# Performance work log

Measured on AMD Instinct MI355X. Metric: run time of the kernel, lower is better.

The kernel has to match this reference:

```python
import jax, jax.numpy as jnp
import numpy as np

B, S, H, I = 2, 2048, 4096, 14336

def setup_inputs() -> dict:
    key = jax.random.key(0)
    k1, k2, k3, k4 = jax.random.split(key, 4)
    sH = 1.0 / np.sqrt(H)
    sI = 1.0 / np.sqrt(I)
    return {
        "x": jax.random.normal(k1, (B, S, H), dtype=jnp.float32),
        "w_gate": jax.random.normal(k2, (I, H), dtype=jnp.float32) * sH,
        "w_up": jax.random.normal(k3, (I, H), dtype=jnp.float32) * sH,
        "w_down": jax.random.normal(k4, (H, I), dtype=jnp.float32) * sI,
    }

def reference(x, w_gate, w_up, w_down):
    # SwiGLU gated MLP: down( silu(x @ Wg^T) * (x @ Wu^T) )
    g = jnp.einsum("bsh,ih->bsi", x, w_gate)   # [B,S,I]
    u = jnp.einsum("bsh,ih->bsi", x, w_up)     # [B,S,I]
    a = jax.nn.silu(g) * u                      # fused silu_mul
    d = jnp.einsum("bsi,hi->bsh", a, w_down)   # [B,S,H]
    return d
```

## Files before the change

kernel.cpp:

```cpp
#include <hip/hip_runtime.h>
#include <hip/hip_bf16.h>
#include <stdint.h>

typedef __bf16 bf16_t;
typedef __bf16 bf16x4 __attribute__((ext_vector_type(4)));
typedef __bf16 bf16x8 __attribute__((ext_vector_type(8)));
typedef float f32x4 __attribute__((ext_vector_type(4)));

#define LDS_CAST(p) ((__attribute__((address_space(3))) void*)(p))
#define GLB_CAST(p) ((const __attribute__((address_space(1))) void*)(p))

__device__ __forceinline__ void gl_lds16(const void* g, void* l) {
  __builtin_amdgcn_global_load_lds(GLB_CAST(g), LDS_CAST(l), 16, 0, 0);
}

#define MFMA16(a,b,c) __builtin_amdgcn_mfma_f32_16x16x32_bf16((a),(b),(c),0,0,0)
#define BARRIER() __builtin_amdgcn_s_barrier()
#define LGKM0() do { asm volatile("s_waitcnt lgkmcnt(0)" ::: "memory"); \
                     __builtin_amdgcn_sched_barrier(0); } while(0)
#define VMW(n)  asm volatile("s_waitcnt vmcnt(" #n ")" ::: "memory")

static constexpr int M_TOT = 4096, H_DIM = 4096, I_DIM = 14336;

__global__ __launch_bounds__(256)
void k_conv(const float4* __restrict__ src, bf16x4* __restrict__ dst, long n4)
{
  long stride = (long)gridDim.x * blockDim.x;
  for (long i = (long)blockIdx.x * blockDim.x + threadIdx.x; i < n4; i += stride) {
    float4 v = src[i];
    bf16x4 o;
    o[0] = (bf16_t)v.x; o[1] = (bf16_t)v.y; o[2] = (bf16_t)v.z; o[3] = (bf16_t)v.w;
    dst[i] = o;
  }
}

__global__ __launch_bounds__(512, 2)
void k_gateup8(const bf16_t* __restrict__ X, const bf16_t* __restrict__ Wg,
               const bf16_t* __restrict__ Wu, bf16_t* __restrict__ Aout)
{
  __shared__ __align__(1024) char lds[131072];
  const int tid = threadIdx.x, wave = tid >> 6, lane = tid & 63;
  const int lr = lane & 15, kg = lane >> 4;
  const int xm = ((lr >> 3) & 1) << 5;
  const int wm = wave >> 2, wn = wave & 3;

  const int bid = blockIdx.x;
  const int swz = (bid & 7) * 224 + (bid >> 3);
  const int tm = swz / 112, tn = swz % 112;

  const int srow  = tid >> 2;
  const int scolb = ((tid & 3) * 16) ^ (((tid >> 5) & 1) << 5);

  const bf16_t* gX = X  + (size_t)(tm * 256 + srow) * H_DIM + (scolb >> 1);
  const bf16_t* gG = Wg + (size_t)(tn * 128 + srow) * H_DIM + (scolb >> 1);
  const bf16_t* gU = Wu + (size_t)(tn * 128 + srow) * H_DIM + (scolb >> 1);
  const size_t xh = (size_t)128 * H_DIM;

  const int offA = (wm * 128 + lr) * 64 + ((kg * 16) ^ xm);
  const int offG = 16384 + (wn * 32 + lr) * 64 + ((kg * 16) ^ xm);
  const int offU = offG + 8192;

  const f32x4 vz = {0.f, 0.f, 0.f, 0.f};
  f32x4 accg[8][2], accu[8][2];
#pragma unroll
  for (int m = 0; m < 8; ++m)
#pragma unroll
    for (int n = 0; n < 2; ++n) { accg[m][n] = vz; accu[m][n] = vz; }

#pragma unroll
  for (int t = 0; t < 3; ++t) {
    char* lb = lds + t * 32768 + wave * 1024;
    gl_lds16(gX + t * 32,      lb);
    gl_lds16(gX + xh + t * 32, lb + 8192);
    gl_lds16(gG + t * 32,      lb + 16384);
    gl_lds16(gU + t * 32,      lb + 24576);
  }
  VMW(8); BARRIER();

  bf16x8 bg[2], bu[2];

#define G1_PHA(bb, DO_STG, sb, kc, VMWAIT)                                    \
  {                                                                           \
    bf16x8 a0[4];                                                             \
    _Pragma("unroll") for (int f = 0; f < 4; ++f)                             \
      a0[f] = *(const bf16x8*)((bb) + offA + f * 1024);                       \
    _Pragma("unroll") for (int n = 0; n < 2; ++n) {                           \
      bg[n] = *(const bf16x8*)((bb) + offG + n * 1024);                       \
      bu[n] = *(const bf16x8*)((bb) + offU + n * 1024); }                     \
    if (DO_STG) { gl_lds16(gX + (kc), (sb));                                  \
                  gl_lds16(gX + xh + (kc), (sb) + 8192); }                    \
    BARRIER(); LGKM0();                                                       \
    __builtin_amdgcn_s_setprio(1);                                            \
    _Pragma("unroll") for (int m = 0; m < 4; ++m)                             \
    _Pragma("unroll") for (int n = 0; n < 2; ++n) {                           \
      accg[m][n] = MFMA16(a0[m], bg[n], accg[m][n]);                          \
      accu[m][n] = MFMA16(a0[m], bu[n], accu[m][n]); }                        \
    __builtin_amdgcn_s_setprio(0);                                            \
    VMWAIT; BARRIER();                                                        \
  }

#define G1_PHB(bb, DO_STG, sb, kc, VMWAIT)                                    \
  {                                                                           \
    bf16x8 a1[4];                                                             \
    _Pragma("unroll") for (int f = 0; f < 4; ++f)                             \
      a1[f] = *(const bf16x8*)((bb) + offA + (f + 4) * 1024);                 \
    if (DO_STG) { gl_lds16(gG + (kc), (sb) + 16384);                          \
                  gl_lds16(gU + (kc), (sb) + 24576); }                        \
    BARRIER(); LGKM0();                                                       \
    __builtin_amdgcn_s_setprio(1);                                            \
    _Pragma("unroll") for (int m = 0; m < 4; ++m)                             \
    _Pragma("unroll") for (int n = 0; n < 2; ++n) {                           \
      accg[4 + m][n] = MFMA16(a1[m], bg[n], accg[4 + m][n]);                  \
      accu[4 + m][n] = MFMA16(a1[m], bu[n], accu[4 + m][n]); }                \
    __builtin_amdgcn_s_setprio(0);                                            \
    VMWAIT; BARRIER();                                                        \
  }

  const int NT = H_DIM / 32;
  for (int T = 0; T < NT - 3; ++T) {
    const char* bb = lds + (T & 3) * 32768;
    char* sb = lds + ((T + 3) & 3) * 32768 + wave * 1024;
    const int kc = (T + 3) * 32;
    G1_PHA(bb, true, sb, kc, VMW(8));
    G1_PHB(bb, true, sb, kc, VMW(8));
  }
  { const char* bb = lds + ((NT-3) & 3) * 32768;
    G1_PHA(bb, false, lds, 0, VMW(4)); G1_PHB(bb, false, lds, 0, VMW(4)); }
  { const char* bb = lds + ((NT-2) & 3) * 32768;
    G1_PHA(bb, false, lds, 0, VMW(0)); G1_PHB(bb, false, lds, 0, VMW(0)); }
  { const char* bb = lds + ((NT-1) & 3) * 32768;
    G1_PHA(bb, false, lds, 0, VMW(0)); G1_PHB(bb, false, lds, 0, VMW(0)); }

  const int r0 = tm * 256 + wm * 128 + kg * 4;
  const int c0 = tn * 128 + wn * 32 + lr;
#pragma unroll
  for (int m = 0; m < 8; ++m)
#pragma unroll
    for (int n = 0; n < 2; ++n)
#pragma unroll
      for (int e = 0; e < 4; ++e) {
        float g = accg[m][n][e];
        float u = accu[m][n][e];
        float s = g / (1.0f + __expf(-g));
        Aout[(size_t)(r0 + m * 16 + e) * I_DIM + c0 + n * 16] = (bf16_t)(s * u);
      }
#undef G1_PHA
#undef G1_PHB
}

__global__ __launch_bounds__(512, 2)
void k_down8(const bf16_t* __restrict__ Aa, const bf16_t* __restrict__ Wd,
             float* __restrict__ D)
{
  __shared__ __align__(1024) char lds[131072];
  const int tid = threadIdx.x, wave = tid >> 6, lane = tid & 63;
  const int lr = lane & 15, kg = lane >> 4;
  const int xm = ((lr >> 3) & 1) << 5;
  const int wm = wave >> 2, wn = wave & 3;

  const int bid = blockIdx.x;
  const int swz = (bid & 7) * 32 + (bid >> 3);
  const int tm = swz >> 4, tn = swz & 15;

  const int srow  = tid >> 2;
  const int scolb = ((tid & 3) * 16) ^ (((tid >> 5) & 1) << 5);

  const bf16_t* gA = Aa + (size_t)(tm * 256 + srow) * I_DIM + (scolb >> 1);
  const bf16_t* gB = Wd + (size_t)(tn * 256 + srow) * I_DIM + (scolb >> 1);
  const size_t hI = (size_t)128 * I_DIM;

  const int offA = (wm * 128 + lr) * 64 + ((kg * 16) ^ xm);
  const int offB = 16384 + (wn * 64 + lr) * 64 + ((kg * 16) ^ xm);

  const f32x4 vz = {0.f, 0.f, 0.f, 0.f};
  f32x4 acc[8][4];
#pragma unroll
  for (int m = 0; m < 8; ++m)
#pragma unroll
    for (int n = 0; n < 4; ++n) acc[m][n] = vz;

#pragma unroll
  for (int t = 0; t < 3; ++t) {
    char* lb = lds + t * 32768 + wave * 1024;
    gl_lds16(gA + t * 32,      lb);
    gl_lds16(gA + hI + t * 32, lb + 8192);
    gl_lds16(gB + t * 32,      lb + 16384);
    gl_lds16(gB + hI + t * 32, lb + 24576);
  }
  VMW(8); BARRIER();

  bf16x8 bfr[4];

#define G2_PHA(bb, DO_STG, sb, kc, VMWAIT)                                    \
  {                                                                           \
    bf16x8 a0[4];                                                             \
    _Pragma("unroll") for (int f = 0; f < 4; ++f)                             \
      a0[f] = *(const bf16x8*)((bb) + offA + f * 1024);                       \
    _Pragma("unroll") for (int n = 0; n < 4; ++n)                             \
      bfr[n] = *(const bf16x8*)((bb) + offB + n * 1024);                      \
    if (DO_STG) { gl_lds16(gA + (kc), (sb));                                  \
                  gl_lds16(gA + hI + (kc), (sb) + 8192); }                    \
    BARRIER(); LGKM0();                                                       \
    __builtin_amdgcn_s_setprio(1);                                            \
    _Pragma("unroll") for (int m = 0; m < 4; ++m)                             \
    _Pragma("unroll") for (int n = 0; n < 4; ++n)                             \
      acc[m][n] = MFMA16(a0[m], bfr[n], acc[m][n]);                           \
    __builtin_amdgcn_s_setprio(0);                                            \
    VMWAIT; BARRIER();                                                        \
  }

#define G2_PHB(bb, DO_STG, sb, kc, VMWAIT)                                    \
  {                                                                           \
    bf16x8 a1[4];                                                             \
    _Pragma("unroll") for (int f = 0; f < 4; ++f)                             \
      a1[f] = *(const bf16x8*)((bb) + offA + (f + 4) * 1024);                 \
    if (DO_STG) { gl_lds16(gB + (kc), (sb) + 16384);                          \
                  gl_lds16(gB + hI + (kc), (sb) + 24576); }                   \
    BARRIER(); LGKM0();                                                       \
    __builtin_amdgcn_s_setprio(1);                                            \
    _Pragma("unroll") for (int m = 0; m < 4; ++m)                             \
    _Pragma("unroll") for (int n = 0; n < 4; ++n)                             \
      acc[4 + m][n] = MFMA16(a1[m], bfr[n], acc[4 + m][n]);                   \
    __builtin_amdgcn_s_setprio(0);                                            \
    VMWAIT; BARRIER();                                                        \
  }

  const int NT = I_DIM / 32;
  for (int T = 0; T < NT - 3; ++T) {
    const char* bb = lds + (T & 3) * 32768;
    char* sb = lds + ((T + 3) & 3) * 32768 + wave * 1024;
    const int kc = (T + 3) * 32;
    G2_PHA(bb, true, sb, kc, VMW(8));
    G2_PHB(bb, true, sb, kc, VMW(8));
  }
  { const char* bb = lds + ((NT-3) & 3) * 32768;
    G2_PHA(bb, false, lds, 0, VMW(4)); G2_PHB(bb, false, lds, 0, VMW(4)); }
  { const char* bb = lds + ((NT-2) & 3) * 32768;
    G2_PHA(bb, false, lds, 0, VMW(0)); G2_PHB(bb, false, lds, 0, VMW(0)); }
  { const char* bb = lds + ((NT-1) & 3) * 32768;
    G2_PHA(bb, false, lds, 0, VMW(0)); G2_PHB(bb, false, lds, 0, VMW(0)); }

  const int r0 = tm * 256 + wm * 128 + kg * 4;
  const int c0 = tn * 256 + wn * 64 + lr;
#pragma unroll
  for (int m = 0; m < 8; ++m)
#pragma unroll
    for (int n = 0; n < 4; ++n)
#pragma unroll
      for (int e = 0; e < 4; ++e)
        D[(size_t)(r0 + m * 16 + e) * H_DIM + c0 + n * 16] = acc[m][n][e];
#undef G2_PHA
#undef G2_PHB
}

extern "C" void kernel_launch(void* const* d_in, const int* in_sizes, int n_in,
                              void* d_out, int out_size, void* d_ws, size_t ws_size,
                              hipStream_t stream) {
  const float* x  = (const float*)d_in[0];
  const float* wg = (const float*)d_in[1];
  const float* wu = (const float*)d_in[2];
  const float* wd = (const float*)d_in[3];
  float* out = (float*)d_out;

  const size_t A_BYTES = (size_t)M_TOT * I_DIM * 2;
  const size_t X_BYTES = (size_t)M_TOT * H_DIM * 2;
  const size_t W_BYTES = (size_t)I_DIM * H_DIM * 2;
  char* ws = (char*)d_ws;
  bf16_t* Ab  = (bf16_t*)(ws);
  bf16_t* Xb  = (bf16_t*)(ws + A_BYTES);
  bf16_t* Wgb = (bf16_t*)(ws + A_BYTES + X_BYTES);
  bf16_t* Wub = (bf16_t*)(ws + A_BYTES + X_BYTES + W_BYTES);
  bf16_t* Wdb = Wgb;

  const long nX = (long)M_TOT * H_DIM / 4;
  const long nW = (long)I_DIM * H_DIM / 4;

  k_conv<<<dim3(2048), dim3(256), 0, stream>>>((const float4*)x,  (bf16x4*)Xb,  nX);
  k_conv<<<dim3(2048), dim3(256), 0, stream>>>((const float4*)wg, (bf16x4*)Wgb, nW);
  k_conv<<<dim3(2048), dim3(256), 0, stream>>>((const float4*)wu, (bf16x4*)Wub, nW);

  k_gateup8<<<dim3(16 * 112), dim3(512), 0, stream>>>(Xb, Wgb, Wub, Ab);

  k_conv<<<dim3(2048), dim3(256), 0, stream>>>((const float4*)wd, (bf16x4*)Wdb, nW);

  k_down8<<<dim3(16 * 16), dim3(512), 0, stream>>>(Ab, Wdb, out);
}
```

Baseline: 1.501 ms.

## Switch both GEMM kernels from 16x16x32 to 32x32x16 bf16 MFMA tiles

Replaces the 16x16x32 MFMA instruction with 32x32x16 in the gate/up and down GEMMs, reorganising per-wave fragments, LDS offsets (the K half is now selected by an XOR on the swizzled offset) and the epilogue row mapping. The K-tile is split into two half-K phases rather than two M-halves. Wait counts are retuned around the new load ordering, with staging issued before the LDS reads. Larger MFMA tiles mean fewer LDS fragment loads and instructions per FLOP, at the cost of a different epilogue store pattern and a changed vmcnt/barrier schedule that could be mistimed.

```diff
diff --git a/kernel.cpp b/kernel.cpp
--- a/kernel.cpp
+++ b/kernel.cpp
@@ -5,7 +5,7 @@
 typedef __bf16 bf16_t;
 typedef __bf16 bf16x4 __attribute__((ext_vector_type(4)));
 typedef __bf16 bf16x8 __attribute__((ext_vector_type(8)));
-typedef float f32x4 __attribute__((ext_vector_type(4)));
+typedef float f32x16 __attribute__((ext_vector_type(16)));
 
 #define LDS_CAST(p) ((__attribute__((address_space(3))) void*)(p))
 #define GLB_CAST(p) ((const __attribute__((address_space(1))) void*)(p))
@@ -14,11 +14,15 @@
   __builtin_amdgcn_global_load_lds(GLB_CAST(g), LDS_CAST(l), 16, 0, 0);
 }
 
-#define MFMA16(a,b,c) __builtin_amdgcn_mfma_f32_16x16x32_bf16((a),(b),(c),0,0,0)
+#define MFMA32(a,b,c) __builtin_amdgcn_mfma_f32_32x32x16_bf16((a),(b),(c),0,0,0)
 #define BARRIER() __builtin_amdgcn_s_barrier()
-#define LGKM0() do { asm volatile("s_waitcnt lgkmcnt(0)" ::: "memory"); \
-                     __builtin_amdgcn_sched_barrier(0); } while(0)
-#define VMW(n)  asm volatile("s_waitcnt vmcnt(" #n ")" ::: "memory")
+#define LGKM0() asm volatile("s_waitcnt lgkmcnt(0)" ::: "memory")
+
+template<int N> __device__ __forceinline__ void vmw() {
+  if constexpr (N == 6)      asm volatile("s_waitcnt vmcnt(6)" ::: "memory");
+  else if constexpr (N == 2) asm volatile("s_waitcnt vmcnt(2)" ::: "memory");
+  else if constexpr (N == 0) asm volatile("s_waitcnt vmcnt(0)" ::: "memory");
+}
 
 static constexpr int M_TOT = 4096, H_DIM = 4096, I_DIM = 14336;
 
@@ -34,14 +38,40 @@
   }
 }
 
+template<int STG, int WAIT>
+__device__ __forceinline__ void g1_phase(
+    const char* bb, int kx, char* sb,
+    const bf16_t* gXk, const bf16_t* gGk, const bf16_t* gUk, size_t xh,
+    int offA, int offG, int offU, f32x16 (&accg)[4], f32x16 (&accu)[4])
+{
+  if constexpr (STG == 1) { gl_lds16(gXk, sb); gl_lds16(gXk + xh, sb + 8192); }
+  if constexpr (STG == 2) { gl_lds16(gGk, sb + 16384); gl_lds16(gUk, sb + 24576); }
+  bf16x8 av[4], bgv, buv;
+#pragma unroll
+  for (int f = 0; f < 4; ++f)
+    av[f] = *(const bf16x8*)(bb + ((offA + f * 2048) ^ kx));
+  bgv = *(const bf16x8*)(bb + (offG ^ kx));
+  buv = *(const bf16x8*)(bb + (offU ^ kx));
+  BARRIER(); LGKM0();
+  __builtin_amdgcn_s_setprio(1);
+#pragma unroll
+  for (int m = 0; m < 4; ++m) {
+    accg[m] = MFMA32(av[m], bgv, accg[m]);
+    accu[m] = MFMA32(av[m], buv, accu[m]);
+  }
+  __builtin_amdgcn_s_setprio(0);
+  vmw<WAIT>();
+  BARRIER();
+}
+
 __global__ __launch_bounds__(512, 2)
 void k_gateup8(const bf16_t* __restrict__ X, const bf16_t* __restrict__ Wg,
                const bf16_t* __restrict__ Wu, bf16_t* __restrict__ Aout)
 {
   __shared__ __align__(1024) char lds[131072];
   const int tid = threadIdx.x, wave = tid >> 6, lane = tid & 63;
-  const int lr = lane & 15, kg = lane >> 4;
-  const int xm = ((lr >> 3) & 1) << 5;
+  const int rowb = lane & 31, hi = lane >> 5;
+  const int xm = ((rowb >> 3) & 1) << 5;
   const int wm = wave >> 2, wn = wave & 3;
 
   const int bid = blockIdx.x;
@@ -56,16 +86,16 @@
   const bf16_t* gU = Wu + (size_t)(tn * 128 + srow) * H_DIM + (scolb >> 1);
   const size_t xh = (size_t)128 * H_DIM;
 
-  const int offA = (wm * 128 + lr) * 64 + ((kg * 16) ^ xm);
-  const int offG = 16384 + (wn * 32 + lr) * 64 + ((kg * 16) ^ xm);
+  const int ck  = (hi * 16) ^ xm;
+  const int offA = (wm * 128 + rowb) * 64 + ck;
+  const int offG = 16384 + (wn * 32 + rowb) * 64 + ck;
   const int offU = offG + 8192;
 
-  const f32x4 vz = {0.f, 0.f, 0.f, 0.f};
-  f32x4 accg[8][2], accu[8][2];
-#pragma unroll
-  for (int m = 0; m < 8; ++m)
-#pragma unroll
-    for (int n = 0; n < 2; ++n) { accg[m][n] = vz; accu[m][n] = vz; }
+  f32x16 accg[4], accu[4];
+#pragma unroll
+  for (int m = 0; m < 4; ++m)
+#pragma unroll
+    for (int r = 0; r < 16; ++r) { accg[m][r] = 0.f; accu[m][r] = 0.f; }
 
 #pragma unroll
   for (int t = 0; t < 3; ++t) {
@@ -75,77 +105,65 @@
     gl_lds16(gG + t * 32,      lb + 16384);
     gl_lds16(gU + t * 32,      lb + 24576);
   }
-  VMW(8); BARRIER();
-
-  bf16x8 bg[2], bu[2];
-
-#define G1_PHA(bb, DO_STG, sb, kc, VMWAIT)                                    \
-  {                                                                           \
-    bf16x8 a0[4];                                                             \
-    _Pragma("unroll") for (int f = 0; f < 4; ++f)                             \
-      a0[f] = *(const bf16x8*)((bb) + offA + f * 1024);                       \
-    _Pragma("unroll") for (int n = 0; n < 2; ++n) {                           \
-      bg[n] = *(const bf16x8*)((bb) + offG + n * 1024);                       \
-      bu[n] = *(const bf16x8*)((bb) + offU + n * 1024); }                     \
-    if (DO_STG) { gl_lds16(gX + (kc), (sb));                                  \
-                  gl_lds16(gX + xh + (kc), (sb) + 8192); }                    \
-    BARRIER(); LGKM0();                                                       \
-    __builtin_amdgcn_s_setprio(1);                                            \
-    _Pragma("unroll") for (int m = 0; m < 4; ++m)                             \
-    _Pragma("unroll") for (int n = 0; n < 2; ++n) {                           \
-      accg[m][n] = MFMA16(a0[m], bg[n], accg[m][n]);                          \
-      accu[m][n] = MFMA16(a0[m], bu[n], accu[m][n]); }                        \
-    __builtin_amdgcn_s_setprio(0);                                            \
-    VMWAIT; BARRIER();                                                        \
-  }
-
-#define G1_PHB(bb, DO_STG, sb, kc, VMWAIT)                                    \
-  {                                                                           \
-    bf16x8 a1[4];                                                             \
-    _Pragma("unroll") for (int f = 0; f < 4; ++f)                             \
-      a1[f] = *(const bf16x8*)((bb) + offA + (f + 4) * 1024);                 \
-    if (DO_STG) { gl_lds16(gG + (kc), (sb) + 16384);                          \
-                  gl_lds16(gU + (kc), (sb) + 24576); }                        \
-    BARRIER(); LGKM0();                                                       \
-    __builtin_amdgcn_s_setprio(1);                                            \
-    _Pragma("unroll") for (int m = 0; m < 4; ++m)                             \
-    _Pragma("unroll") for (int n = 0; n < 2; ++n) {                           \
-      accg[4 + m][n] = MFMA16(a1[m], bg[n], accg[4 + m][n]);                  \
-      accu[4 + m][n] = MFMA16(a1[m], bu[n], accu[4 + m][n]); }                \
-    __builtin_amdgcn_s_setprio(0);                                            \
-    VMWAIT; BARRIER();                                                        \
-  }
+  vmw<8 - 2>(); BARRIER();
 
   const int NT = H_DIM / 32;
   for (int T = 0; T < NT - 3; ++T) {
     const char* bb = lds + (T & 3) * 32768;
     char* sb = lds + ((T + 3) & 3) * 32768 + wave * 1024;
     const int kc = (T + 3) * 32;
-    G1_PHA(bb, true, sb, kc, VMW(8));
-    G1_PHB(bb, true, sb, kc, VMW(8));
-  }
-  { const char* bb = lds + ((NT-3) & 3) * 32768;
-    G1_PHA(bb, false, lds, 0, VMW(4)); G1_PHB(bb, false, lds, 0, VMW(4)); }
-  { const char* bb = lds + ((NT-2) & 3) * 32768;
-    G1_PHA(bb, false, lds, 0, VMW(0)); G1_PHB(bb, false, lds, 0, VMW(0)); }
-  { const char* bb = lds + ((NT-1) & 3) * 32768;
-    G1_PHA(bb, false, lds, 0, VMW(0)); G1_PHB(bb, false, lds, 0, VMW(0)); }
-
-  const int r0 = tm * 256 + wm * 128 + kg * 4;
-  const int c0 = tn * 128 + wn * 32 + lr;
-#pragma unroll
-  for (int m = 0; m < 8; ++m)
+    g1_phase<1, -1>(bb, 0,  sb, gX + kc, gG + kc, gU + kc, xh, offA, offG, offU, accg, accu);
+    g1_phase<2,  6>(bb, 32, sb, gX + kc, gG + kc, gU + kc, xh, offA, offG, offU, accg, accu);
+  }
+  { const char* bb = lds + ((NT - 3) & 3) * 32768;
+    g1_phase<0, -1>(bb, 0, lds, gX, gG, gU, xh, offA, offG, offU, accg, accu);
+    g1_phase<0,  2>(bb, 32, lds, gX, gG, gU, xh, offA, offG, offU, accg, accu); }
+  { const char* bb = lds + ((NT - 2) & 3) * 32768;
+    g1_phase<0, -1>(bb, 0, lds, gX, gG, gU, xh, offA, offG, offU, accg, accu);
+    g1_phase<0,  0>(bb, 32, lds, gX, gG, gU, xh, offA, offG, offU, accg, accu); }
+  { const char* bb = lds + ((NT - 1) & 3) * 32768;
+    g1_phase<0, -1>(bb, 0, lds, gX, gG, gU, xh, offA, offG, offU, accg, accu);
+    g1_phase<0, -1>(bb, 32, lds, gX, gG, gU, xh, offA, offG, offU, accg, accu); }
+
+  const int r0 = tm * 256 + wm * 128 + 4 * hi;
+  const int c0 = tn * 128 + wn * 32 + rowb;
+#pragma unroll
+  for (int m = 0; m < 4; ++m)
+#pragma unroll
+    for (int r = 0; r < 16; ++r) {
+      const int row = r0 + m * 32 + (r & 3) + 8 * (r >> 2);
+      float g = accg[m][r];
+      float u = accu[m][r];
+      float s = g / (1.0f + __expf(-g));
+      Aout[(size_t)row * I_DIM + c0] = (bf16_t)(s * u);
+    }
+}
+
+template<int STG, int WAIT>
+__device__ __forceinline__ void g2_phase(
+    const char* bb, int kx, char* sb,
+    const bf16_t* gAk, const bf16_t* gBk, size_t hI,
+    int offA, int offB, f32x16 (&acc)[4][2])
+{
+  if constexpr (STG == 1) { gl_lds16(gAk, sb); gl_lds16(gAk + hI, sb + 8192); }
+  if constexpr (STG == 2) { gl_lds16(gBk, sb + 16384); gl_lds16(gBk + hI, sb + 24576); }
+  bf16x8 av[4], bv[2];
+#pragma unroll
+  for (int f = 0; f < 4; ++f)
+    av[f] = *(const bf16x8*)(bb + ((offA + f * 2048) ^ kx));
+#pragma unroll
+  for (int n = 0; n < 2; ++n)
+    bv[n] = *(const bf16x8*)(bb + ((offB + n * 2048) ^ kx));
+  BARRIER(); LGKM0();
+  __builtin_amdgcn_s_setprio(1);
+#pragma unroll
+  for (int m = 0; m < 4; ++m)
 #pragma unroll
     for (int n = 0; n < 2; ++n)
-#pragma unroll
-      for (int e = 0; e < 4; ++e) {
-        float g = accg[m][n][e];
-        float u = accu[m][n][e];
-        float s = g / (1.0f + __expf(-g));
-        Aout[(size_t)(r0 + m * 16 + e) * I_DIM + c0 + n * 16] = (bf16_t)(s * u);
-      }
-#undef G1_PHA
-#undef G1_PHB
+      acc[m][n] = MFMA32(av[m], bv[n], acc[m][n]);
+  __builtin_amdgcn_s_setprio(0);
+  vmw<WAIT>();
+  BARRIER();
 }
 
 __global__ __launch_bounds__(512, 2)
@@ -154,8 +172,8 @@
 {
   __shared__ __align__(1024) char lds[131072];
   const int tid = threadIdx.x, wave = tid >> 6, lane = tid & 63;
-  const int lr = lane & 15, kg = lane >> 4;
-  const int xm = ((lr >> 3) & 1) << 5;
+  const int rowb = lane & 31, hi = lane >> 5;
+  const int xm = ((rowb >> 3) & 1) << 5;
   const int wm = wave >> 2, wn = wave & 3;
 
   const int bid = blockIdx.x;
@@ -169,15 +187,17 @@
   const bf16_t* gB = Wd + (size_t)(tn * 256 + srow) * I_DIM + (scolb >> 1);
   const size_t hI = (size_t)128 * I_DIM;
 
-  const int offA = (wm * 128 + lr) * 64 + ((kg * 16) ^ xm);
-  const int offB = 16384 + (wn * 64 + lr) * 64 + ((kg * 16) ^ xm);
-
-  const f32x4 vz = {0.f, 0.f, 0.f, 0.f};
-  f32x4 acc[8][4];
-#pragma unroll
-  for (int m = 0; m < 8; ++m)
-#pragma unroll
-    for (int n = 0; n < 4; ++n) acc[m][n] = vz;
+  const int ck  = (hi * 16) ^ xm;
+  const int offA = (wm * 128 + rowb) * 64 + ck;
+  const int offB = 16384 + (wn * 64 + rowb) * 64 + ck;
+
+  f32x16 acc[4][2];
+#pragma unroll
+  for (int m = 0; m < 4; ++m)
+#pragma unroll
+    for (int n = 0; n < 2; ++n)
+#pragma unroll
+      for (int r = 0; r < 16; ++r) acc[m][n][r] = 0.f;
 
 #pragma unroll
   for (int t = 0; t < 3; ++t) {
@@ -187,70 +207,37 @@
     gl_lds16(gB + t * 32,      lb + 16384);
     gl_lds16(gB + hI + t * 32, lb + 24576);
   }
-  VMW(8); BARRIER();
-
-  bf16x8 bfr[4];
-
-#define G2_PHA(bb, DO_STG, sb, kc, VMWAIT)                                    \
-  {                                                                           \
-    bf16x8 a0[4];                                                             \
-    _Pragma("unroll") for (int f = 0; f < 4; ++f)                             \
-      a0[f] = *(const bf16x8*)((bb) + offA + f * 1024);                       \
-    _Pragma("unroll") for (int n = 0; n < 4; ++n)                             \
-      bfr[n] = *(const bf16x8*)((bb) + offB + n * 1024);                      \
-    if (DO_STG) { gl_lds16(gA + (kc), (sb));                                  \
-                  gl_lds16(gA + hI + (kc), (sb) + 8192); }                    \
-    BARRIER(); LGKM0();                                                       \
-    __builtin_amdgcn_s_setprio(1);                                            \
-    _Pragma("unroll") for (int m = 0; m < 4; ++m)                             \
-    _Pragma("unroll") for (int n = 0; n < 4; ++n)                             \
-      acc[m][n] = MFMA16(a0[m], bfr[n], acc[m][n]);                           \
-    __builtin_amdgcn_s_setprio(0);                                            \
-    VMWAIT; BARRIER();                                                        \
-  }
-
-#define G2_PHB(bb, DO_STG, sb, kc, VMWAIT)                                    \
-  {                                                                           \
-    bf16x8 a1[4];                                                             \
-    _Pragma("unroll") for (int f = 0; f < 4; ++f)                             \
-      a1[f] = *(const bf16x8*)((bb) + offA + (f + 4) * 1024);                 \
-    if (DO_STG) { gl_lds16(gB + (kc), (sb) + 16384);                          \
-                  gl_lds16(gB + hI + (kc), (sb) + 24576); }                   \
-    BARRIER(); LGKM0();                                                       \
-    __builtin_amdgcn_s_setprio(1);                                            \
-    _Pragma("unroll") for (int m = 0; m < 4; ++m)                             \
-    _Pragma("unroll") for (int n = 0; n < 4; ++n)                             \
-      acc[4 + m][n] = MFMA16(a1[m], bfr[n], acc[4 + m][n]);                   \
-    __builtin_amdgcn_s_setprio(0);                                            \
-    VMWAIT; BARRIER();                                                        \
-  }
+  vmw<6>(); BARRIER();
 
   const int NT = I_DIM / 32;
   for (int T = 0; T < NT - 3; ++T) {
     const char* bb = lds + (T & 3) * 32768;
     char* sb = lds + ((T + 3) & 3) * 32768 + wave * 1024;
     const int kc = (T + 3) * 32;
-    G2_PHA(bb, true, sb, kc, VMW(8));
-    G2_PHB(bb, true, sb, kc, VMW(8));
-  }
-  { const char* bb = lds + ((NT-3) & 3) * 32768;
-    G2_PHA(bb, false, lds, 0, VMW(4)); G2_PHB(bb, false, lds, 0, VMW(4)); }
-  { const char* bb = lds + ((NT-2) & 3) * 32768;
-    G2_PHA(bb, false, lds, 0, VMW(0)); G2_PHB(bb, false, lds, 0, VMW(0)); }
-  { const char* bb = lds + ((NT-1) & 3) * 32768;
-    G2_PHA(bb, false, lds, 0, VMW(0)); G2_PHB(bb, false, lds, 0, VMW(0)); }
-
-  const int r0 = tm * 256 + wm * 128 + kg * 4;
-  const int c0 = tn * 256 + wn * 64 + lr;
-#pragma unroll
-  for (int m = 0; m < 8; ++m)
-#pragma unroll
-    for (int n = 0; n < 4; ++n)
-#pragma unroll
-      for (int e = 0; e < 4; ++e)
-        D[(size_t)(r0 + m * 16 + e) * H_DIM + c0 + n * 16] = acc[m][n][e];
-#undef G2_PHA
-#undef G2_PHB
+    g2_phase<1, -1>(bb, 0,  sb, gA + kc, gB + kc, hI, offA, offB, acc);
+    g2_phase<2,  6>(bb, 32, sb, gA + kc, gB + kc, hI, offA, offB, acc);
+  }
+  { const char* bb = lds + ((NT - 3) & 3) * 32768;
+    g2_phase<0, -1>(bb, 0, lds, gA, gB, hI, offA, offB, acc);
+    g2_phase<0,  2>(bb, 32, lds, gA, gB, hI, offA, offB, acc); }
+  { const char* bb = lds + ((NT - 2) & 3) * 32768;
+    g2_phase<0, -1>(bb, 0, lds, gA, gB, hI, offA, offB, acc);
+    g2_phase<0,  0>(bb, 32, lds, gA, gB, hI, offA, offB, acc); }
+  { const char* bb = lds + ((NT - 1) & 3) * 32768;
+    g2_phase<0, -1>(bb, 0, lds, gA, gB, hI, offA, offB, acc);
+    g2_phase<0, -1>(bb, 32, lds, gA, gB, hI, offA, offB, acc); }
+
+  const int r0 = tm * 256 + wm * 128 + 4 * hi;
+  const int c0 = tn * 256 + wn * 64 + rowb;
+#pragma unroll
+  for (int m = 0; m < 4; ++m)
+#pragma unroll
+    for (int n = 0; n < 2; ++n)
+#pragma unroll
+      for (int r = 0; r < 16; ++r) {
+        const int row = r0 + m * 32 + (r & 3) + 8 * (r >> 2);
+        D[(size_t)row * H_DIM + c0 + n * 32] = acc[m][n][r];
+      }
 }
 
 extern "C" void kernel_launch(void* const* d_in, const int* in_sizes, int n_in,
```

New measurement: 1.651 ms. 1.1x slower.

## Collapse two half-phase K-steps into one tile step with a single barrier

Applied to the files above, without the earlier changes.

Both GEMM kernels drop the split into A/B half-phases, each of which had two barriers and an explicit lgkmcnt(0) wait. Each K-tile now issues all four global-to-LDS prefetches up front, reads all A and B fragments, runs all MFMAs, and ends with one vmcnt wait and one barrier. The aim is to cut barrier and wait stalls per K step. In exchange it uses more registers for fragments, and vmcnt(6) waits for more than strictly needed, which shortens the effective prefetch depth. The block-to-tile mapping is also changed so that consecutive blocks within each group of eight share the same weight column tile while iterating over the row tiles.

```diff
diff --git a/kernel.cpp b/kernel.cpp
--- a/kernel.cpp
+++ b/kernel.cpp
@@ -16,9 +16,13 @@
 
 #define MFMA16(a,b,c) __builtin_amdgcn_mfma_f32_16x16x32_bf16((a),(b),(c),0,0,0)
 #define BARRIER() __builtin_amdgcn_s_barrier()
-#define LGKM0() do { asm volatile("s_waitcnt lgkmcnt(0)" ::: "memory"); \
-                     __builtin_amdgcn_sched_barrier(0); } while(0)
-#define VMW(n)  asm volatile("s_waitcnt vmcnt(" #n ")" ::: "memory")
+
+template<int N> __device__ __forceinline__ void vmw() {
+  if constexpr (N == 8)      asm volatile("s_waitcnt vmcnt(8)" ::: "memory");
+  else if constexpr (N == 6) asm volatile("s_waitcnt vmcnt(6)" ::: "memory");
+  else if constexpr (N == 4) asm volatile("s_waitcnt vmcnt(4)" ::: "memory");
+  else if constexpr (N == 0) asm volatile("s_waitcnt vmcnt(0)" ::: "memory");
+}
 
 static constexpr int M_TOT = 4096, H_DIM = 4096, I_DIM = 14336;
 
@@ -45,8 +49,9 @@
   const int wm = wave >> 2, wn = wave & 3;
 
   const int bid = blockIdx.x;
-  const int swz = (bid & 7) * 224 + (bid >> 3);
-  const int tm = swz / 112, tn = swz % 112;
+  const int i8  = bid >> 3;
+  const int tn  = (bid & 7) * 14 + (i8 >> 4);
+  const int tm  = i8 & 15;
 
   const int srow  = tid >> 2;
   const int scolb = ((tid & 3) * 16) ^ (((tid >> 5) & 1) << 5);
@@ -56,8 +61,9 @@
   const bf16_t* gU = Wu + (size_t)(tn * 128 + srow) * H_DIM + (scolb >> 1);
   const size_t xh = (size_t)128 * H_DIM;
 
-  const int offA = (wm * 128 + lr) * 64 + ((kg * 16) ^ xm);
-  const int offG = 16384 + (wn * 32 + lr) * 64 + ((kg * 16) ^ xm);
+  const int ck   = (kg * 16) ^ xm;
+  const int offA = (wm * 128 + lr) * 64 + ck;
+  const int offG = 16384 + (wn * 32 + lr) * 64 + ck;
   const int offU = offG + 8192;
 
   const f32x4 vz = {0.f, 0.f, 0.f, 0.f};
@@ -75,61 +81,42 @@
     gl_lds16(gG + t * 32,      lb + 16384);
     gl_lds16(gU + t * 32,      lb + 24576);
   }
-  VMW(8); BARRIER();
-
-  bf16x8 bg[2], bu[2];
-
-#define G1_PHA(bb, DO_STG, sb, kc, VMWAIT)                                    \
-  {                                                                           \
-    bf16x8 a0[4];                                                             \
-    _Pragma("unroll") for (int f = 0; f < 4; ++f)                             \
-      a0[f] = *(const bf16x8*)((bb) + offA + f * 1024);                       \
-    _Pragma("unroll") for (int n = 0; n < 2; ++n) {                           \
-      bg[n] = *(const bf16x8*)((bb) + offG + n * 1024);                       \
-      bu[n] = *(const bf16x8*)((bb) + offU + n * 1024); }                     \
-    if (DO_STG) { gl_lds16(gX + (kc), (sb));                                  \
-                  gl_lds16(gX + xh + (kc), (sb) + 8192); }                    \
-    BARRIER(); LGKM0();                                                       \
-    __builtin_amdgcn_s_setprio(1);                                            \
-    _Pragma("unroll") for (int m = 0; m < 4; ++m)                             \
-    _Pragma("unroll") for (int n = 0; n < 2; ++n) {                           \
-      accg[m][n] = MFMA16(a0[m], bg[n], accg[m][n]);                          \
-      accu[m][n] = MFMA16(a0[m], bu[n], accu[m][n]); }                        \
-    __builtin_amdgcn_s_setprio(0);                                            \
-    VMWAIT; BARRIER();                                                        \
-  }
-
-#define G1_PHB(bb, DO_STG, sb, kc, VMWAIT)                                    \
-  {                                                                           \
-    bf16x8 a1[4];                                                             \
-    _Pragma("unroll") for (int f = 0; f < 4; ++f)                             \
-      a1[f] = *(const bf16x8*)((bb) + offA + (f + 4) * 1024);                 \
-    if (DO_STG) { gl_lds16(gG + (kc), (sb) + 16384);                          \
-                  gl_lds16(gU + (kc), (sb) + 24576); }                        \
-    BARRIER(); LGKM0();                                                       \
-    __builtin_amdgcn_s_setprio(1);                                            \
-    _Pragma("unroll") for (int m = 0; m < 4; ++m)                             \
-    _Pragma("unroll") for (int n = 0; n < 2; ++n) {                           \
-      accg[4 + m][n] = MFMA16(a1[m], bg[n], accg[4 + m][n]);                  \
-      accu[4 + m][n] = MFMA16(a1[m], bu[n], accu[4 + m][n]); }                \
-    __builtin_amdgcn_s_setprio(0);                                            \
-    VMWAIT; BARRIER();                                                        \
+  vmw<8>(); BARRIER();
+
+#define G1_TILE(T, DO_STG, WAITN, DO_BAR)                                    \
+  {                                                                          \
+    const char* bb = lds + (((T) & 3) << 15);                                \
+    if (DO_STG) {                                                            \
+      char* sb = lds + ((((T) + 3) & 3) << 15) + wave * 1024;                \
+      const int kc = ((T) + 3) * 32;                                         \
+      gl_lds16(gX + kc,      sb);                                            \
+      gl_lds16(gX + xh + kc, sb + 8192);                                     \
+      gl_lds16(gG + kc,      sb + 16384);                                    \
+      gl_lds16(gU + kc,      sb + 24576);                                    \
+    }                                                                        \
+    bf16x8 bg[2], bu[2], a[8];                                               \
+    _Pragma("unroll") for (int n = 0; n < 2; ++n) {                          \
+      bg[n] = *(const bf16x8*)(bb + offG + n * 1024);                        \
+      bu[n] = *(const bf16x8*)(bb + offU + n * 1024); }                      \
+    _Pragma("unroll") for (int f = 0; f < 8; ++f)                            \
+      a[f] = *(const bf16x8*)(bb + offA + f * 1024);                         \
+    __builtin_amdgcn_s_setprio(1);                                           \
+    _Pragma("unroll") for (int m = 0; m < 8; ++m)                            \
+    _Pragma("unroll") for (int n = 0; n < 2; ++n) {                          \
+      accg[m][n] = MFMA16(a[m], bg[n], accg[m][n]);                          \
+      accu[m][n] = MFMA16(a[m], bu[n], accu[m][n]); }                        \
+    __builtin_amdgcn_s_setprio(0);                                           \
+    vmw<WAITN>();                                                            \
+    if (DO_BAR) BARRIER();                                                   \
   }
 
   const int NT = H_DIM / 32;
-  for (int T = 0; T < NT - 3; ++T) {
-    const char* bb = lds + (T & 3) * 32768;
-    char* sb = lds + ((T + 3) & 3) * 32768 + wave * 1024;
-    const int kc = (T + 3) * 32;
-    G1_PHA(bb, true, sb, kc, VMW(8));
-    G1_PHB(bb, true, sb, kc, VMW(8));
-  }
-  { const char* bb = lds + ((NT-3) & 3) * 32768;
-    G1_PHA(bb, false, lds, 0, VMW(4)); G1_PHB(bb, false, lds, 0, VMW(4)); }
-  { const char* bb = lds + ((NT-2) & 3) * 32768;
-    G1_PHA(bb, false, lds, 0, VMW(0)); G1_PHB(bb, false, lds, 0, VMW(0)); }
-  { const char* bb = lds + ((NT-1) & 3) * 32768;
-    G1_PHA(bb, false, lds, 0, VMW(0)); G1_PHB(bb, false, lds, 0, VMW(0)); }
+  for (int T = 0; T <= NT - 4; ++T)
+    G1_TILE(T, true, 6, true);
+  G1_TILE(NT - 3, false, 4, true);
+  G1_TILE(NT - 2, false, 0, true);
+  G1_TILE(NT - 1, false, 8 , false);
+#undef G1_TILE
 
   const int r0 = tm * 256 + wm * 128 + kg * 4;
   const int c0 = tn * 128 + wn * 32 + lr;
@@ -144,8 +131,6 @@
         float s = g / (1.0f + __expf(-g));
         Aout[(size_t)(r0 + m * 16 + e) * I_DIM + c0 + n * 16] = (bf16_t)(s * u);
       }
-#undef G1_PHA
-#undef G1_PHB
 }
 
 __global__ __launch_bounds__(512, 2)
@@ -159,8 +144,9 @@
   const int wm = wave >> 2, wn = wave & 3;
 
   const int bid = blockIdx.x;
-  const int swz = (bid & 7) * 32 + (bid >> 3);
-  const int tm = swz >> 4, tn = swz & 15;
+  const int i8  = bid >> 3;
+  const int tn  = (bid & 7) * 2 + (i8 >> 4);
+  const int tm  = i8 & 15;
 
   const int srow  = tid >> 2;
   const int scolb = ((tid & 3) * 16) ^ (((tid >> 5) & 1) << 5);
@@ -169,8 +155,9 @@
   const bf16_t* gB = Wd + (size_t)(tn * 256 + srow) * I_DIM + (scolb >> 1);
   const size_t hI = (size_t)128 * I_DIM;
 
-  const int offA = (wm * 128 + lr) * 64 + ((kg * 16) ^ xm);
-  const int offB = 16384 + (wn * 64 + lr) * 64 + ((kg * 16) ^ xm);
+  const int ck   = (kg * 16) ^ xm;
+  const int offA = (wm * 128 + lr) * 64 + ck;
+  const int offB = 16384 + (wn * 64 + lr) * 64 + ck;
 
   const f32x4 vz = {0.f, 0.f, 0.f, 0.f};
   f32x4 acc[8][4];
@@ -187,58 +174,40 @@
     gl_lds16(gB + t * 32,      lb + 16384);
     gl_lds16(gB + hI + t * 32, lb + 24576);
   }
-  VMW(8); BARRIER();
-
-  bf16x8 bfr[4];
-
-#define G2_PHA(bb, DO_STG, sb, kc, VMWAIT)                                    \
-  {                                                                           \
-    bf16x8 a0[4];                                                             \
-    _Pragma("unroll") for (int f = 0; f < 4; ++f)                             \
-      a0[f] = *(const bf16x8*)((bb) + offA + f * 1024);                       \
-    _Pragma("unroll") for (int n = 0; n < 4; ++n)                             \
-      bfr[n] = *(const bf16x8*)((bb) + offB + n * 1024);                      \
-    if (DO_STG) { gl_lds16(gA + (kc), (sb));                                  \
-                  gl_lds16(gA + hI + (kc), (sb) + 8192); }                    \
-    BARRIER(); LGKM0();                                                       \
-    __builtin_amdgcn_s_setprio(1);                                            \
-    _Pragma("unroll") for (int m = 0; m < 4; ++m)                             \
-    _Pragma("unroll") for (int n = 0; n < 4; ++n)                             \
-      acc[m][n] = MFMA16(a0[m], bfr[n], acc[m][n]);                           \
-    __builtin_amdgcn_s_setprio(0);                                            \
-    VMWAIT; BARRIER();                                                        \
-  }
-
-#define G2_PHB(bb, DO_STG, sb, kc, VMWAIT)                                    \
-  {                                                                           \
-    bf16x8 a1[4];                                                             \
-    _Pragma("unroll") for (int f = 0; f < 4; ++f)                             \
-      a1[f] = *(const bf16x8*)((bb) + offA + (f + 4) * 1024);                 \
-    if (DO_STG) { gl_lds16(gB + (kc), (sb) + 16384);                          \
-                  gl_lds16(gB + hI + (kc), (sb) + 24576); }                   \
-    BARRIER(); LGKM0();                                                       \
-    __builtin_amdgcn_s_setprio(1);                                            \
-    _Pragma("unroll") for (int m = 0; m < 4; ++m)                             \
-    _Pragma("unroll") for (int n = 0; n < 4; ++n)                             \
-      acc[4 + m][n] = MFMA16(a1[m], bfr[n], acc[4 + m][n]);                   \
-    __builtin_amdgcn_s_setprio(0);                                            \
-    VMWAIT; BARRIER();                                                        \
+  vmw<8>(); BARRIER();
+
+#define G2_TILE(T, DO_STG, WAITN, DO_BAR)                                    \
+  {                                                                          \
+    const char* bb = lds + (((T) & 3) << 15);                                \
+    if (DO_STG) {                                                            \
+      char* sb = lds + ((((T) + 3) & 3) << 15) + wave * 1024;                \
+      const int kc = ((T) + 3) * 32;                                         \
+      gl_lds16(gA + kc,      sb);                                            \
+      gl_lds16(gA + hI + kc, sb + 8192);                                     \
+      gl_lds16(gB + kc,      sb + 16384);                                    \
+      gl_lds16(gB + hI + kc, sb + 24576);                                    \
+    }                                                                        \
+    bf16x8 b[4], a[8];                                                       \
+    _Pragma("unroll") for (int n = 0; n < 4; ++n)                            \
+      b[n] = *(const bf16x8*)(bb + offB + n * 1024);                         \
+    _Pragma("unroll") for (int f = 0; f < 8; ++f)                            \
+      a[f] = *(const bf16x8*)(bb + offA + f * 1024);                         \
+    __builtin_amdgcn_s_setprio(1);                                           \
+    _Pragma("unroll") for (int m = 0; m < 8; ++m)                            \
+    _Pragma("unroll") for (int n = 0; n < 4; ++n)                            \
+      acc[m][n] = MFMA16(a[m], b[n], acc[m][n]);                             \
+    __builtin_amdgcn_s_setprio(0);                                           \
+    vmw<WAITN>();                                                            \
+    if (DO_BAR) BARRIER();                                                   \
   }
 
   const int NT = I_DIM / 32;
-  for (int T = 0; T < NT - 3; ++T) {
-    const char* bb = lds + (T & 3) * 32768;
-    char* sb = lds + ((T + 3) & 3) * 32768 + wave * 1024;
-    const int kc = (T + 3) * 32;
-    G2_PHA(bb, true, sb, kc, VMW(8));
-    G2_PHB(bb, true, sb, kc, VMW(8));
-  }
-  { const char* bb = lds + ((NT-3) & 3) * 32768;
-    G2_PHA(bb, false, lds, 0, VMW(4)); G2_PHB(bb, false, lds, 0, VMW(4)); }
-  { const char* bb = lds + ((NT-2) & 3) * 32768;
-    G2_PHA(bb, false, lds, 0, VMW(0)); G2_PHB(bb, false, lds, 0, VMW(0)); }
-  { const char* bb = lds + ((NT-1) & 3) * 32768;
-    G2_PHA(bb, false, lds, 0, VMW(0)); G2_PHB(bb, false, lds, 0, VMW(0)); }
+  for (int T = 0; T <= NT - 4; ++T)
+    G2_TILE(T, true, 6, true);
+  G2_TILE(NT - 3, false, 4, true);
+  G2_TILE(NT - 2, false, 0, true);
+  G2_TILE(NT - 1, false, 8, false);
+#undef G2_TILE
 
   const int r0 = tm * 256 + wm * 128 + kg * 4;
   const int c0 = tn * 256 + wn * 64 + lr;
@@ -249,8 +218,6 @@
 #pragma unroll
       for (int e = 0; e < 4; ++e)
         D[(size_t)(r0 + m * 16 + e) * H_DIM + c0 + n * 16] = acc[m][n][e];
-#undef G2_PHA
-#undef G2_PHB
 }
 
 extern "C" void kernel_launch(void* const* d_in, const int* in_sizes, int n_in,
```

After: 1.439 ms. 1.04x faster.
